# Kernel tuning notes

Measured on AMD Instinct MI355X. Metric: run time of the kernel, lower is better.

The kernel has to match this reference:

```python
import jax, jax.numpy as jnp
import numpy as np

NUM_HEADS = 8
IN_DIM = 384
HEAD_DIM = IN_DIM // NUM_HEADS  # 48


def setup_inputs() -> dict:
    key = jax.random.key(0)
    ks = jax.random.split(key, 6)
    B, N, M, C = 4, 4096, 1024, 384
    q_x = jax.random.normal(ks[0], (B, N, C), dtype=jnp.float32)
    kv_x = jax.random.normal(ks[1], (B, M, C), dtype=jnp.float32)
    s = C ** -0.5  # fan-in style init scale
    Wq = jax.random.normal(ks[2], (C, IN_DIM), dtype=jnp.float32) * s
    Wkv = jax.random.normal(ks[3], (C, 2 * IN_DIM), dtype=jnp.float32) * s
    Wproj = jax.random.normal(ks[4], (IN_DIM, IN_DIM), dtype=jnp.float32) * (IN_DIM ** -0.5)
    bproj = jnp.zeros((IN_DIM,), dtype=jnp.float32)
    return {"q_x": q_x, "kv_x": kv_x, "Wq": Wq, "Wkv": Wkv, "Wproj": Wproj, "bproj": bproj}


def reference(q_x, kv_x, Wq, Wkv, Wproj, bproj):
    B, N, C = q_x.shape
    M = kv_x.shape[1]
    scale = HEAD_DIM ** -0.5
    # q: [B, H, N, hd]
    q = (q_x @ Wq).reshape(B, N, NUM_HEADS, HEAD_DIM).transpose(0, 2, 1, 3)
    # k, v: [B, H, M, hd]
    kv = (kv_x @ Wkv).reshape(B, M, 2, NUM_HEADS, HEAD_DIM).transpose(2, 0, 3, 1, 4)
    k, v = kv[0], kv[1]
    # attention scores [B, H, N, M]
    attn = jax.nn.softmax(jnp.einsum('bhnd,bhmd->bhnm', q, k) * scale, axis=-1)
    x = jnp.einsum('bhnm,bhmd->bhnd', attn, v)  # [B, H, N, hd]
    x = x.transpose(0, 2, 1, 3).reshape(B, N, IN_DIM)
    x = x @ Wproj + bproj
    # sr_ratio == 1 residual: add raw q projection back
    q_res = q.transpose(0, 2, 1, 3).reshape(B, N, IN_DIM)
    return q_res + x
```

## Files before the change

kernel.cpp:

```cpp
#include <hip/hip_runtime.h>
#include <hip/hip_bf16.h>
#include <math.h>

#define B_ 4
#define N_ 4096
#define M_ 1024
#define C_ 384
#define NH_ 8
#define HD_ 48

typedef float f32x4 __attribute__((ext_vector_type(4)));
typedef float f32x16 __attribute__((ext_vector_type(16)));
typedef short bf16x8 __attribute__((ext_vector_type(8)));

typedef __attribute__((address_space(3))) unsigned int lds_uint;
typedef const __attribute__((address_space(1))) unsigned int glob_uint;

__device__ __forceinline__ void gld_lds16(const void* g, void* l) {
    __builtin_amdgcn_global_load_lds((glob_uint*)g, (lds_uint*)l, 16, 0, 0);
}

__device__ __forceinline__ unsigned short f2bf(float x) {
    unsigned int u = __builtin_bit_cast(unsigned int, x);
    return (unsigned short)((u + 0x7FFFu + ((u >> 16) & 1u)) >> 16);
}
__device__ __forceinline__ float bf2f(unsigned short x) {
    return __builtin_bit_cast(float, (unsigned int)x << 16);
}
__device__ __forceinline__ float fast_exp2(float x) {
#if __has_builtin(__builtin_amdgcn_exp2f)
    return __builtin_amdgcn_exp2f(x);
#else
    return exp2f(x);
#endif
}
__device__ __forceinline__ uint2 pack4_rne(float a, float b, float c, float d) {
    uint2 r;
    r.x = (unsigned int)f2bf(a) | ((unsigned int)f2bf(b) << 16);
    r.y = (unsigned int)f2bf(c) | ((unsigned int)f2bf(d) << 16);
    return r;
}

#define QSCALE 0.20823490983597203f
#define INV_QSCALE (1.0f / 0.20823490983597203f)

__global__ __launch_bounds__(256)
void prep(const float* __restrict__ qx_f, unsigned short* __restrict__ qx_bf,
          const float* __restrict__ kvx_f, unsigned short* __restrict__ kvx_bf,
          const float* __restrict__ Wq, const float* __restrict__ Wkv,
          const float* __restrict__ Wproj,
          unsigned short* __restrict__ Wq_t, unsigned short* __restrict__ Wkv_t,
          unsigned short* __restrict__ Wproj_t)
{
    __shared__ unsigned short T[64 * 72];
    const int tid = threadIdx.x;
    int bid = blockIdx.x;

    if (bid < 7680) {
        size_t i4 = (size_t)bid * 256 + tid;
        const float* src; unsigned short* dst;
        if (i4 < 1572864u) { src = qx_f; dst = qx_bf; }
        else { src = kvx_f; dst = kvx_bf; i4 -= 1572864u; }
        float4 v = *(const float4*)&src[i4 * 4];
        *(uint2*)&dst[i4 * 4] = pack4_rne(v.x, v.y, v.z, v.w);
        return;
    }

    bid -= 7680;
    const float* W; unsigned short* Wt; int N, kt, nt;
    if (bid < 36)       { W = Wq;    Wt = Wq_t;    N = 384; kt = bid / 6;  nt = bid - kt * 6; }
    else if (bid < 108) { bid -= 36;  W = Wkv;   Wt = Wkv_t;   N = 768; kt = bid / 12; nt = bid - kt * 12; }
    else                { bid -= 108; W = Wproj; Wt = Wproj_t; N = 384; kt = bid / 6;  nt = bid - kt * 6; }
    const int k0 = kt * 64, n0 = nt * 64;

    #pragma unroll
    for (int it = 0; it < 4; ++it) {
        int k = it * 16 + (tid >> 4);
        int n4 = (tid & 15) * 4;
        float4 v = *(const float4*)&W[(size_t)(k0 + k) * N + n0 + n4];
        T[(n4 + 0) * 72 + k] = f2bf(v.x);
        T[(n4 + 1) * 72 + k] = f2bf(v.y);
        T[(n4 + 2) * 72 + k] = f2bf(v.z);
        T[(n4 + 3) * 72 + k] = f2bf(v.w);
    }
    __syncthreads();
    #pragma unroll
    for (int i = 0; i < 2; ++i) {
        int s = tid + 256 * i;
        int n = s >> 3, part = s & 7;
        *(uint4*)&Wt[(size_t)(n0 + n) * C_ + k0 + part * 8] = *(const uint4*)&T[n * 72 + part * 8];
    }
}

__device__ __forceinline__ void stage128(const unsigned short* src, unsigned short* lds,
                                         int kk, int tid) {
    #pragma unroll
    for (int r = 0; r < 4; ++r) {
        int off = r * 256 + tid;
        int row = off >> 3;
        int c = off & 7;
        int gc = c ^ (row & 7);
        gld_lds16(src + (size_t)row * C_ + kk + gc * 8, lds + (size_t)off * 8);
    }
}
__device__ __forceinline__ bf16x8 frag_ld(const unsigned short* lds, int row, int chunk) {
    return *(const bf16x8*)&lds[row * 64 + ((chunk ^ (row & 7)) << 3)];
}

#define GEMM_CORE(Aptr, Wptr)                                                        \
    f32x4 acc[4][4];                                                                 \
    _Pragma("unroll")                                                                \
    for (int rt = 0; rt < 4; ++rt)                                                   \
        _Pragma("unroll")                                                            \
        for (int ct = 0; ct < 4; ++ct) acc[rt][ct] = (f32x4){0.f, 0.f, 0.f, 0.f};    \
    const int wrow0 = (wave & 1) * 64;                                               \
    const int wcol0 = (wave >> 1) * 64;                                              \
    for (int kk = 0; kk < C_; kk += 64) {                                            \
        __syncthreads();                                                             \
        stage128(Aptr, As, kk, tid);                                                 \
        stage128(Wptr, Ws, kk, tid);                                                 \
        __syncthreads();                                                             \
        _Pragma("unroll")                                                            \
        for (int ks = 0; ks < 2; ++ks) {                                             \
            bf16x8 af[4], wf[4];                                                     \
            _Pragma("unroll")                                                        \
            for (int rt = 0; rt < 4; ++rt)                                           \
                af[rt] = frag_ld(As, wrow0 + rt * 16 + ln, ks * 4 + quad);           \
            _Pragma("unroll")                                                        \
            for (int ct = 0; ct < 4; ++ct)                                           \
                wf[ct] = frag_ld(Ws, wcol0 + ct * 16 + ln, ks * 4 + quad);           \
            _Pragma("unroll")                                                        \
            for (int rt = 0; rt < 4; ++rt)                                           \
                _Pragma("unroll")                                                    \
                for (int ct = 0; ct < 4; ++ct)                                       \
                    acc[rt][ct] = __builtin_amdgcn_mfma_f32_16x16x32_bf16(           \
                        wf[ct], af[rt], acc[rt][ct], 0, 0, 0);                       \
        }                                                                            \
    }

__global__ __launch_bounds__(256)
void gemm_qkv(const unsigned short* __restrict__ qx, const unsigned short* __restrict__ kvx,
              const unsigned short* __restrict__ Wqt, const unsigned short* __restrict__ Wkvt,
              unsigned short* __restrict__ qbf,
              unsigned short* __restrict__ kbf, unsigned short* __restrict__ vbf)
{
    __shared__ unsigned short As[128 * 64];
    __shared__ unsigned short Ws[128 * 64];
    const int tid = threadIdx.x;
    const int wave = tid >> 6;
    const int lane = tid & 63;
    const int ln = lane & 15;
    const int quad = lane >> 4;

    int bid = blockIdx.x;
    int mode, row0, col0;
    const unsigned short *A, *Wt;
    if (bid < 384) { mode = 0; A = qx;  Wt = Wqt;  row0 = (bid / 3) * 128; col0 = (bid % 3) * 128; }
    else { bid -= 384; mode = 1; A = kvx; Wt = Wkvt; row0 = (bid / 6) * 128; col0 = (bid % 6) * 128; }

    GEMM_CORE(A + (size_t)row0 * C_, Wt + (size_t)col0 * C_)

    #pragma unroll
    for (int rt = 0; rt < 4; ++rt) {
        int grow = row0 + wrow0 + rt * 16 + ln;
        #pragma unroll
        for (int ct = 0; ct < 4; ++ct) {
            int col = col0 + wcol0 + ct * 16 + quad * 4;
            f32x4 v = acc[rt][ct];
            if (mode == 0) {
                int b = grow >> 12, n = grow & (N_ - 1);
                int h = col / HD_, d = col - h * HD_;
                *(uint2*)&qbf[(((size_t)(b * NH_ + h) * N_) + n) * HD_ + d] =
                    pack4_rne(v[0] * QSCALE, v[1] * QSCALE, v[2] * QSCALE, v[3] * QSCALE);
            } else {
                int b = grow >> 10, m = grow & (M_ - 1);
                if (col < C_) {
                    int h = col / HD_, d = col - h * HD_;
                    *(uint2*)&kbf[(((size_t)(b * NH_ + h) * M_) + m) * HD_ + d] =
                        pack4_rne(v[0], v[1], v[2], v[3]);
                } else {
                    int c2 = col - C_;
                    int h = c2 / HD_, d = c2 - h * HD_;
                    size_t base = ((size_t)(b * NH_ + h) * HD_ + d) * M_ + m;
                    #pragma unroll
                    for (int r = 0; r < 4; ++r) vbf[base + (size_t)r * M_] = f2bf(v[r]);
                }
            }
        }
    }
}

__global__ __launch_bounds__(256)
void gemm_out(const unsigned short* __restrict__ A, const unsigned short* __restrict__ Wt,
              float* __restrict__ out0,
              const unsigned short* __restrict__ qbf, const float* __restrict__ bias)
{
    __shared__ unsigned short As[128 * 64];
    __shared__ unsigned short Ws[128 * 64];
    const int tid = threadIdx.x;
    const int wave = tid >> 6;
    const int lane = tid & 63;
    const int ln = lane & 15;
    const int quad = lane >> 4;
    const int row0 = (blockIdx.x / 3) * 128;
    const int col0 = (blockIdx.x % 3) * 128;

    GEMM_CORE(A + (size_t)row0 * C_, Wt + (size_t)col0 * C_)

    #pragma unroll
    for (int rt = 0; rt < 4; ++rt) {
        int grow = row0 + wrow0 + rt * 16 + ln;
        #pragma unroll
        for (int ct = 0; ct < 4; ++ct) {
            int col = col0 + wcol0 + ct * 16 + quad * 4;
            f32x4 v = acc[rt][ct];
            size_t idx = (size_t)grow * C_ + col;
            int b = grow >> 12, n = grow & (N_ - 1);
            int h = col / HD_, d = col - h * HD_;
            uint2 ad = *(const uint2*)&qbf[(((size_t)(b * NH_ + h) * N_) + n) * HD_ + d];
            float4 bi = *(const float4*)&bias[col];
            float4 o;
            o.x = v[0] + bf2f((unsigned short)(ad.x & 0xFFFF)) * INV_QSCALE + bi.x;
            o.y = v[1] + bf2f((unsigned short)(ad.x >> 16))    * INV_QSCALE + bi.y;
            o.z = v[2] + bf2f((unsigned short)(ad.y & 0xFFFF)) * INV_QSCALE + bi.z;
            o.w = v[3] + bf2f((unsigned short)(ad.y >> 16))    * INV_QSCALE + bi.w;
            *(float4*)&out0[idx] = o;
        }
    }
}

__global__ __launch_bounds__(256, 2)
void attn_mfma(const unsigned short* __restrict__ qbf,
               const unsigned short* __restrict__ kbf,
               const unsigned short* __restrict__ vbf,
               unsigned short* __restrict__ of)
{
    const int tid = threadIdx.x;
    const int wave = tid >> 6;
    const int lane = tid & 63;
    const int l31 = lane & 31;
    const int hi  = lane >> 5;
    const int bh = blockIdx.x;
    const int n0w = blockIdx.y * 256 + wave * 64;

    const unsigned short* kb = kbf + (size_t)bh * M_ * HD_;
    const unsigned short* vb = vbf + (size_t)bh * HD_ * M_;

    bf16x8 qb[2][3];
    #pragma unroll
    for (int qt = 0; qt < 2; ++qt) {
        const unsigned short* qp = qbf + ((size_t)bh * N_ + n0w + qt * 32 + l31) * HD_;
        #pragma unroll
        for (int s = 0; s < 3; ++s)
            qb[qt][s] = *(const bf16x8*)(qp + s * 16 + hi * 8);
    }

    f32x16 O[2][2];
    #pragma unroll
    for (int qt = 0; qt < 2; ++qt)
        #pragma unroll
        for (int ot2 = 0; ot2 < 2; ++ot2)
            #pragma unroll
            for (int r = 0; r < 16; ++r) O[qt][ot2][r] = 0.f;
    float rs[2] = {0.f, 0.f};

    for (int mtt = 0; mtt < 32; ++mtt) {
        const int m0 = mtt * 32;

        bf16x8 ka[3];
        #pragma unroll
        for (int s = 0; s < 3; ++s)
            ka[s] = *(const bf16x8*)&kb[(size_t)(m0 + l31) * HD_ + s * 16 + hi * 8];

        bf16x8 va[2][2];
        #pragma unroll
        for (int ot2 = 0; ot2 < 2; ++ot2)
            #pragma unroll
            for (int s2 = 0; s2 < 2; ++s2)
                va[ot2][s2] = *(const bf16x8*)&vb[(size_t)(ot2 * 32 + l31) * M_ + m0 + s2 * 16 + hi * 8];

        #pragma unroll
        for (int qt = 0; qt < 2; ++qt) {
            f32x16 S;
            #pragma unroll
            for (int r = 0; r < 16; ++r) S[r] = 0.f;
            #pragma unroll
            for (int s = 0; s < 3; ++s)
                S = __builtin_amdgcn_mfma_f32_32x32x16_bf16(ka[s], qb[qt][s], S, 0, 0, 0);

            float p[16];
            #pragma unroll
            for (int r = 0; r < 16; ++r) p[r] = fast_exp2(S[r]);
            {
                float s0 = (p[0] + p[1]) + (p[2] + p[3]);
                float s1 = (p[4] + p[5]) + (p[6] + p[7]);
                float s2 = (p[8] + p[9]) + (p[10] + p[11]);
                float s3 = (p[12] + p[13]) + (p[14] + p[15]);
                rs[qt] += (s0 + s1) + (s2 + s3);
            }

            unsigned c0[4], c1[4];
            #pragma unroll
            for (int g = 0; g < 4; ++g) {
                c0[g] = (__builtin_bit_cast(unsigned int, p[4 * g + 0]) >> 16) |
                        (__builtin_bit_cast(unsigned int, p[4 * g + 1]) & 0xFFFF0000u);
                c1[g] = (__builtin_bit_cast(unsigned int, p[4 * g + 2]) >> 16) |
                        (__builtin_bit_cast(unsigned int, p[4 * g + 3]) & 0xFFFF0000u);
            }

            #pragma unroll
            for (int s2 = 0; s2 < 2; ++s2) {
                unsigned o00 = c0[2 * s2], o01 = c0[2 * s2 + 1];
                unsigned o10 = c1[2 * s2], o11 = c1[2 * s2 + 1];
                unsigned pr0 = (unsigned)__shfl_xor((int)(hi ? o00 : o01), 32);
                unsigned pr1 = (unsigned)__shfl_xor((int)(hi ? o10 : o11), 32);
                unsigned d0 = hi ? pr0 : o00;
                unsigned d1 = hi ? pr1 : o10;
                unsigned d2 = hi ? o01 : pr0;
                unsigned d3 = hi ? o11 : pr1;
                uint4 u = {d0, d1, d2, d3};
                bf16x8 pf = __builtin_bit_cast(bf16x8, u);
                #pragma unroll
                for (int ot2 = 0; ot2 < 2; ++ot2)
                    O[qt][ot2] = __builtin_amdgcn_mfma_f32_32x32x16_bf16(
                        va[ot2][s2], pf, O[qt][ot2], 0, 0, 0);
            }
        }
    }

    float inv[2];
    #pragma unroll
    for (int qt = 0; qt < 2; ++qt) {
        float x = rs[qt] + __shfl_xor(rs[qt], 32);
        inv[qt] = 1.0f / x;
    }

    const int b = bh >> 3, h = bh & 7;
    #pragma unroll
    for (int qt = 0; qt < 2; ++qt) {
        size_t grow = (size_t)b * N_ + n0w + qt * 32 + l31;
        unsigned short* orow = of + grow * C_ + h * HD_;
        #pragma unroll
        for (int ot2 = 0; ot2 < 2; ++ot2) {
            const int rgmax = (ot2 == 0) ? 4 : 2;
            #pragma unroll
            for (int rg = 0; rg < 4; ++rg) {
                if (rg >= rgmax) continue;
                int d0 = ot2 * 32 + rg * 8 + hi * 4;
                *(uint2*)(orow + d0) = pack4_rne(
                    O[qt][ot2][rg * 4 + 0] * inv[qt], O[qt][ot2][rg * 4 + 1] * inv[qt],
                    O[qt][ot2][rg * 4 + 2] * inv[qt], O[qt][ot2][rg * 4 + 3] * inv[qt]);
            }
        }
    }
}

extern "C" void kernel_launch(void* const* d_in, const int* in_sizes, int n_in,
                              void* d_out, int out_size, void* d_ws, size_t ws_size,
                              hipStream_t stream) {
    const float* q_x   = (const float*)d_in[0];
    const float* kv_x  = (const float*)d_in[1];
    const float* Wq    = (const float*)d_in[2];
    const float* Wkv   = (const float*)d_in[3];
    const float* Wproj = (const float*)d_in[4];
    const float* bproj = (const float*)d_in[5];
    float* out = (float*)d_out;

    unsigned short* qbf     = (unsigned short*)d_ws;
    unsigned short* kbf     = qbf     + 6291456;
    unsigned short* vbf     = kbf     + 1572864;
    unsigned short* of      = vbf     + 1572864;
    unsigned short* qx_bf   = of      + 6291456;
    unsigned short* kvx_bf  = qx_bf   + 6291456;
    unsigned short* Wq_t    = kvx_bf  + 1572864;
    unsigned short* Wkv_t   = Wq_t    + 147456;
    unsigned short* Wproj_t = Wkv_t   + 294912;

    dim3 blk(256);

    prep<<<dim3(7824), blk, 0, stream>>>(q_x, qx_bf, kv_x, kvx_bf,
                                         Wq, Wkv, Wproj, Wq_t, Wkv_t, Wproj_t);

    gemm_qkv<<<dim3(576), blk, 0, stream>>>(
        qx_bf, kvx_bf, Wq_t, Wkv_t, qbf, kbf, vbf);

    attn_mfma<<<dim3(32, 16), blk, 0, stream>>>(qbf, kbf, vbf, of);

    gemm_out<<<dim3(384), blk, 0, stream>>>(of, Wproj_t, out, qbf, bproj);
}
```

Baseline: 168.8 us.

## Double-buffer LDS tiles in projection GEMMs to overlap loads with MFMA

The shared GEMM core used by the QKV and output projections now keeps two LDS buffers for the A and W tiles. The next K-slice is prefetched with global_load_lds while MFMAs run on the current one, and there is one barrier per iteration instead of two. The aim is to hide global-to-LDS latency behind compute. This doubles LDS use per block to 64KB, which may lower occupancy.

```diff
diff --git a/kernel.cpp b/kernel.cpp
--- a/kernel.cpp
+++ b/kernel.cpp
@@ -115,20 +115,25 @@
         for (int ct = 0; ct < 4; ++ct) acc[rt][ct] = (f32x4){0.f, 0.f, 0.f, 0.f};    \
     const int wrow0 = (wave & 1) * 64;                                               \
     const int wcol0 = (wave >> 1) * 64;                                              \
-    for (int kk = 0; kk < C_; kk += 64) {                                            \
-        __syncthreads();                                                             \
-        stage128(Aptr, As, kk, tid);                                                 \
-        stage128(Wptr, Ws, kk, tid);                                                 \
-        __syncthreads();                                                             \
+    stage128(Aptr, &As[0][0], 0, tid);                                               \
+    stage128(Wptr, &Ws[0][0], 0, tid);                                               \
+    asm volatile("s_waitcnt vmcnt(0)" ::: "memory");                                 \
+    __builtin_amdgcn_s_barrier();                                                    \
+    for (int kt = 0; kt < 6; ++kt) {                                                 \
+        const int cur = kt & 1;                                                      \
+        if (kt < 5) {                                                                \
+            stage128(Aptr, &As[cur ^ 1][0], (kt + 1) * 64, tid);                     \
+            stage128(Wptr, &Ws[cur ^ 1][0], (kt + 1) * 64, tid);                     \
+        }                                                                            \
         _Pragma("unroll")                                                            \
         for (int ks = 0; ks < 2; ++ks) {                                             \
             bf16x8 af[4], wf[4];                                                     \
             _Pragma("unroll")                                                        \
             for (int rt = 0; rt < 4; ++rt)                                           \
-                af[rt] = frag_ld(As, wrow0 + rt * 16 + ln, ks * 4 + quad);           \
+                af[rt] = frag_ld(&As[cur][0], wrow0 + rt * 16 + ln, ks * 4 + quad);  \
             _Pragma("unroll")                                                        \
             for (int ct = 0; ct < 4; ++ct)                                           \
-                wf[ct] = frag_ld(Ws, wcol0 + ct * 16 + ln, ks * 4 + quad);           \
+                wf[ct] = frag_ld(&Ws[cur][0], wcol0 + ct * 16 + ln, ks * 4 + quad);  \
             _Pragma("unroll")                                                        \
             for (int rt = 0; rt < 4; ++rt)                                           \
                 _Pragma("unroll")                                                    \
@@ -136,6 +141,10 @@
                     acc[rt][ct] = __builtin_amdgcn_mfma_f32_16x16x32_bf16(           \
                         wf[ct], af[rt], acc[rt][ct], 0, 0, 0);                       \
         }                                                                            \
+        asm volatile("s_waitcnt vmcnt(0)" ::: "memory");                             \
+        __builtin_amdgcn_sched_barrier(0);                                           \
+        __builtin_amdgcn_s_barrier();                                                \
+        __builtin_amdgcn_sched_barrier(0);                                           \
     }
 
 __global__ __launch_bounds__(256)
@@ -144,8 +153,8 @@
               unsigned short* __restrict__ qbf,
               unsigned short* __restrict__ kbf, unsigned short* __restrict__ vbf)
 {
-    __shared__ unsigned short As[128 * 64];
-    __shared__ unsigned short Ws[128 * 64];
+    __shared__ unsigned short As[2][128 * 64];
+    __shared__ unsigned short Ws[2][128 * 64];
     const int tid = threadIdx.x;
     const int wave = tid >> 6;
     const int lane = tid & 63;
@@ -195,8 +204,8 @@
               float* __restrict__ out0,
               const unsigned short* __restrict__ qbf, const float* __restrict__ bias)
 {
-    __shared__ unsigned short As[128 * 64];
-    __shared__ unsigned short Ws[128 * 64];
+    __shared__ unsigned short As[2][128 * 64];
+    __shared__ unsigned short Ws[2][128 * 64];
     const int tid = threadIdx.x;
     const int wave = tid >> 6;
     const int lane = tid & 63;
```

Result: no change. 169.5 us (+0.4%).

## Split attention key range across wave pairs and combine partial outputs in LDS

Applied to the files above, without the earlier changes.

Each attention block now covers 128 queries instead of 256. Two waves share each 64-query tile, and each wave processes half of the 1024 keys. The second wave writes its partial O accumulators and row sums to shared memory, and the first wave adds them in before normalizing. The query range is covered by two back-to-back launches offset by a y0 parameter, and the launch bound is raised to 4 blocks per SM. The aim is to shorten the per-wave serial key loop and raise occupancy, at the cost of an LDS reduction, a block barrier, an extra launch and tighter register limits that could cause spills.

```diff
diff --git a/kernel.cpp b/kernel.cpp
--- a/kernel.cpp
+++ b/kernel.cpp
@@ -229,19 +229,23 @@
     }
 }
 
-__global__ __launch_bounds__(256, 2)
+__global__ __launch_bounds__(256, 4)
 void attn_mfma(const unsigned short* __restrict__ qbf,
                const unsigned short* __restrict__ kbf,
                const unsigned short* __restrict__ vbf,
-               unsigned short* __restrict__ of)
+               unsigned short* __restrict__ of, int y0)
 {
+    __shared__ float comb[2][64][72];
+
     const int tid = threadIdx.x;
     const int wave = tid >> 6;
+    const int qpair = wave >> 1;
+    const int mhalf = wave & 1;
     const int lane = tid & 63;
     const int l31 = lane & 31;
     const int hi  = lane >> 5;
     const int bh = blockIdx.x;
-    const int n0w = blockIdx.y * 256 + wave * 64;
+    const int n0w = (blockIdx.y + y0) * 128 + qpair * 64;
 
     const unsigned short* kb = kbf + (size_t)bh * M_ * HD_;
     const unsigned short* vb = vbf + (size_t)bh * HD_ * M_;
@@ -264,7 +268,8 @@
             for (int r = 0; r < 16; ++r) O[qt][ot2][r] = 0.f;
     float rs[2] = {0.f, 0.f};
 
-    for (int mtt = 0; mtt < 32; ++mtt) {
+    const int mtt0 = mhalf * 16;
+    for (int mtt = mtt0; mtt < mtt0 + 16; ++mtt) {
         const int m0 = mtt * 32;
 
         bf16x8 ka[3];
@@ -328,6 +333,29 @@
         }
     }
 
+    if (mhalf) {
+        float* ex = &comb[qpair][lane][0];
+        *(f32x16*)&ex[0]  = O[0][0];
+        *(f32x16*)&ex[16] = O[0][1];
+        *(f32x16*)&ex[32] = O[1][0];
+        *(f32x16*)&ex[48] = O[1][1];
+        ex[64] = rs[0];
+        ex[65] = rs[1];
+    }
+    __syncthreads();
+    if (mhalf) return;
+
+    {
+        const float* ex = &comb[qpair][lane][0];
+        f32x16 u00 = *(const f32x16*)&ex[0];
+        f32x16 u01 = *(const f32x16*)&ex[16];
+        f32x16 u10 = *(const f32x16*)&ex[32];
+        f32x16 u11 = *(const f32x16*)&ex[48];
+        O[0][0] += u00; O[0][1] += u01; O[1][0] += u10; O[1][1] += u11;
+        rs[0] += ex[64];
+        rs[1] += ex[65];
+    }
+
     float inv[2];
     #pragma unroll
     for (int qt = 0; qt < 2; ++qt) {
@@ -384,7 +412,8 @@
     gemm_qkv<<<dim3(576), blk, 0, stream>>>(
         qx_bf, kvx_bf, Wq_t, Wkv_t, qbf, kbf, vbf);
 
-    attn_mfma<<<dim3(32, 16), blk, 0, stream>>>(qbf, kbf, vbf, of);
+    attn_mfma<<<dim3(32, 16), blk, 0, stream>>>(qbf, kbf, vbf, of, 0);
+    attn_mfma<<<dim3(32, 16), blk, 0, stream>>>(qbf, kbf, vbf, of, 16);
 
     gemm_out<<<dim3(384), blk, 0, stream>>>(of, Wproj_t, out, qbf, bproj);
 }
```

After: 353.1 us. 2.09x slower.

## Double-buffer K/V loads in attention and halve output GEMM column tile

Applied to the files above, without the earlier changes.

The attention loop now prefetches the next 32-key K/V fragment set into registers while computing the current one, ping-ponging between two register buffers, and wraps the MFMA groups in s_setprio to favour matrix issue. The output projection GEMM switches from 128x128 to 128x64 tiles, doubling the grid to 768 blocks for better CU occupancy. The costs are extra register pressure in attention, which may hurt occupancy at the 2-block launch bound, and more redundant A-tile loads in the output GEMM.

```diff
diff --git a/kernel.cpp b/kernel.cpp
--- a/kernel.cpp
+++ b/kernel.cpp
@@ -96,6 +96,17 @@
                                          int kk, int tid) {
     #pragma unroll
     for (int r = 0; r < 4; ++r) {
+        int off = r * 256 + tid;
+        int row = off >> 3;
+        int c = off & 7;
+        int gc = c ^ (row & 7);
+        gld_lds16(src + (size_t)row * C_ + kk + gc * 8, lds + (size_t)off * 8);
+    }
+}
+__device__ __forceinline__ void stage64(const unsigned short* src, unsigned short* lds,
+                                        int kk, int tid) {
+    #pragma unroll
+    for (int r = 0; r < 2; ++r) {
         int off = r * 256 + tid;
         int row = off >> 3;
         int c = off & 7;
@@ -196,22 +207,53 @@
               const unsigned short* __restrict__ qbf, const float* __restrict__ bias)
 {
     __shared__ unsigned short As[128 * 64];
-    __shared__ unsigned short Ws[128 * 64];
+    __shared__ unsigned short Ws[64 * 64];
     const int tid = threadIdx.x;
     const int wave = tid >> 6;
     const int lane = tid & 63;
     const int ln = lane & 15;
     const int quad = lane >> 4;
-    const int row0 = (blockIdx.x / 3) * 128;
-    const int col0 = (blockIdx.x % 3) * 128;
-
-    GEMM_CORE(A + (size_t)row0 * C_, Wt + (size_t)col0 * C_)
+    const int row0 = (blockIdx.x / 6) * 128;
+    const int col0 = (blockIdx.x % 6) * 64;
+    const int wrow0 = (wave & 1) * 64;
+    const int wcol0 = (wave >> 1) * 32;
+
+    f32x4 acc[4][2];
+    #pragma unroll
+    for (int rt = 0; rt < 4; ++rt)
+        #pragma unroll
+        for (int ct = 0; ct < 2; ++ct) acc[rt][ct] = (f32x4){0.f, 0.f, 0.f, 0.f};
+
+    const unsigned short* Ap = A + (size_t)row0 * C_;
+    const unsigned short* Wp = Wt + (size_t)col0 * C_;
+    for (int kk = 0; kk < C_; kk += 64) {
+        __syncthreads();
+        stage128(Ap, As, kk, tid);
+        stage64(Wp, Ws, kk, tid);
+        __syncthreads();
+        #pragma unroll
+        for (int ks = 0; ks < 2; ++ks) {
+            bf16x8 af[4], wf[2];
+            #pragma unroll
+            for (int rt = 0; rt < 4; ++rt)
+                af[rt] = frag_ld(As, wrow0 + rt * 16 + ln, ks * 4 + quad);
+            #pragma unroll
+            for (int ct = 0; ct < 2; ++ct)
+                wf[ct] = frag_ld(Ws, wcol0 + ct * 16 + ln, ks * 4 + quad);
+            #pragma unroll
+            for (int rt = 0; rt < 4; ++rt)
+                #pragma unroll
+                for (int ct = 0; ct < 2; ++ct)
+                    acc[rt][ct] = __builtin_amdgcn_mfma_f32_16x16x32_bf16(
+                        wf[ct], af[rt], acc[rt][ct], 0, 0, 0);
+        }
+    }
 
     #pragma unroll
     for (int rt = 0; rt < 4; ++rt) {
         int grow = row0 + wrow0 + rt * 16 + ln;
         #pragma unroll
-        for (int ct = 0; ct < 4; ++ct) {
+        for (int ct = 0; ct < 2; ++ct) {
             int col = col0 + wcol0 + ct * 16 + quad * 4;
             f32x4 v = acc[rt][ct];
             size_t idx = (size_t)grow * C_ + col;
@@ -229,6 +271,78 @@
     }
 }
 
+__device__ __forceinline__ void attn_load(bf16x8 (&ka)[3], bf16x8 (&va)[2][2],
+                                          const unsigned short* kb,
+                                          const unsigned short* vb,
+                                          int m0, int l31, int hi)
+{
+    #pragma unroll
+    for (int s = 0; s < 3; ++s)
+        ka[s] = *(const bf16x8*)&kb[(size_t)(m0 + l31) * HD_ + s * 16 + hi * 8];
+    #pragma unroll
+    for (int ot2 = 0; ot2 < 2; ++ot2)
+        #pragma unroll
+        for (int s2 = 0; s2 < 2; ++s2)
+            va[ot2][s2] = *(const bf16x8*)&vb[(size_t)(ot2 * 32 + l31) * M_ + m0 + s2 * 16 + hi * 8];
+}
+
+__device__ __forceinline__ void attn_compute(const bf16x8 (&ka)[3], const bf16x8 (&va)[2][2],
+                                             const bf16x8 (&qb)[2][3],
+                                             f32x16 (&O)[2][2], float (&rs)[2], int hi)
+{
+    #pragma unroll
+    for (int qt = 0; qt < 2; ++qt) {
+        f32x16 S;
+        #pragma unroll
+        for (int r = 0; r < 16; ++r) S[r] = 0.f;
+        __builtin_amdgcn_s_setprio(1);
+        #pragma unroll
+        for (int s = 0; s < 3; ++s)
+            S = __builtin_amdgcn_mfma_f32_32x32x16_bf16(ka[s], qb[qt][s], S, 0, 0, 0);
+        __builtin_amdgcn_s_setprio(0);
+
+        float p[16];
+        #pragma unroll
+        for (int r = 0; r < 16; ++r) p[r] = fast_exp2(S[r]);
+        {
+            float s0 = (p[0] + p[1]) + (p[2] + p[3]);
+            float s1 = (p[4] + p[5]) + (p[6] + p[7]);
+            float s2 = (p[8] + p[9]) + (p[10] + p[11]);
+            float s3 = (p[12] + p[13]) + (p[14] + p[15]);
+            rs[qt] += (s0 + s1) + (s2 + s3);
+        }
+
+        unsigned c0[4], c1[4];
+        #pragma unroll
+        for (int g = 0; g < 4; ++g) {
+            c0[g] = (__builtin_bit_cast(unsigned int, p[4 * g + 0]) >> 16) |
+                    (__builtin_bit_cast(unsigned int, p[4 * g + 1]) & 0xFFFF0000u);
+            c1[g] = (__builtin_bit_cast(unsigned int, p[4 * g + 2]) >> 16) |
+                    (__builtin_bit_cast(unsigned int, p[4 * g + 3]) & 0xFFFF0000u);
+        }
+
+        #pragma unroll
+        for (int s2 = 0; s2 < 2; ++s2) {
+            unsigned o00 = c0[2 * s2], o01 = c0[2 * s2 + 1];
+            unsigned o10 = c1[2 * s2], o11 = c1[2 * s2 + 1];
+            unsigned pr0 = (unsigned)__shfl_xor((int)(hi ? o00 : o01), 32);
+            unsigned pr1 = (unsigned)__shfl_xor((int)(hi ? o10 : o11), 32);
+            unsigned d0 = hi ? pr0 : o00;
+            unsigned d1 = hi ? pr1 : o10;
+            unsigned d2 = hi ? o01 : pr0;
+            unsigned d3 = hi ? o11 : pr1;
+            uint4 u = {d0, d1, d2, d3};
+            bf16x8 pf = __builtin_bit_cast(bf16x8, u);
+            __builtin_amdgcn_s_setprio(1);
+            #pragma unroll
+            for (int ot2 = 0; ot2 < 2; ++ot2)
+                O[qt][ot2] = __builtin_amdgcn_mfma_f32_32x32x16_bf16(
+                    va[ot2][s2], pf, O[qt][ot2], 0, 0, 0);
+            __builtin_amdgcn_s_setprio(0);
+        }
+    }
+}
+
 __global__ __launch_bounds__(256, 2)
 void attn_mfma(const unsigned short* __restrict__ qbf,
                const unsigned short* __restrict__ kbf,
@@ -264,68 +378,15 @@
             for (int r = 0; r < 16; ++r) O[qt][ot2][r] = 0.f;
     float rs[2] = {0.f, 0.f};
 
-    for (int mtt = 0; mtt < 32; ++mtt) {
-        const int m0 = mtt * 32;
-
-        bf16x8 ka[3];
-        #pragma unroll
-        for (int s = 0; s < 3; ++s)
-            ka[s] = *(const bf16x8*)&kb[(size_t)(m0 + l31) * HD_ + s * 16 + hi * 8];
-
-        bf16x8 va[2][2];
-        #pragma unroll
-        for (int ot2 = 0; ot2 < 2; ++ot2)
-            #pragma unroll
-            for (int s2 = 0; s2 < 2; ++s2)
-                va[ot2][s2] = *(const bf16x8*)&vb[(size_t)(ot2 * 32 + l31) * M_ + m0 + s2 * 16 + hi * 8];
-
-        #pragma unroll
-        for (int qt = 0; qt < 2; ++qt) {
-            f32x16 S;
-            #pragma unroll
-            for (int r = 0; r < 16; ++r) S[r] = 0.f;
-            #pragma unroll
-            for (int s = 0; s < 3; ++s)
-                S = __builtin_amdgcn_mfma_f32_32x32x16_bf16(ka[s], qb[qt][s], S, 0, 0, 0);
-
-            float p[16];
-            #pragma unroll
-            for (int r = 0; r < 16; ++r) p[r] = fast_exp2(S[r]);
-            {
-                float s0 = (p[0] + p[1]) + (p[2] + p[3]);
-                float s1 = (p[4] + p[5]) + (p[6] + p[7]);
-                float s2 = (p[8] + p[9]) + (p[10] + p[11]);
-                float s3 = (p[12] + p[13]) + (p[14] + p[15]);
-                rs[qt] += (s0 + s1) + (s2 + s3);
-            }
-
-            unsigned c0[4], c1[4];
-            #pragma unroll
-            for (int g = 0; g < 4; ++g) {
-                c0[g] = (__builtin_bit_cast(unsigned int, p[4 * g + 0]) >> 16) |
-                        (__builtin_bit_cast(unsigned int, p[4 * g + 1]) & 0xFFFF0000u);
-                c1[g] = (__builtin_bit_cast(unsigned int, p[4 * g + 2]) >> 16) |
-                        (__builtin_bit_cast(unsigned int, p[4 * g + 3]) & 0xFFFF0000u);
-            }
-
-            #pragma unroll
-            for (int s2 = 0; s2 < 2; ++s2) {
-                unsigned o00 = c0[2 * s2], o01 = c0[2 * s2 + 1];
-                unsigned o10 = c1[2 * s2], o11 = c1[2 * s2 + 1];
-                unsigned pr0 = (unsigned)__shfl_xor((int)(hi ? o00 : o01), 32);
-                unsigned pr1 = (unsigned)__shfl_xor((int)(hi ? o10 : o11), 32);
-                unsigned d0 = hi ? pr0 : o00;
-                unsigned d1 = hi ? pr1 : o10;
-                unsigned d2 = hi ? o01 : pr0;
-                unsigned d3 = hi ? o11 : pr1;
-                uint4 u = {d0, d1, d2, d3};
-                bf16x8 pf = __builtin_bit_cast(bf16x8, u);
-                #pragma unroll
-                for (int ot2 = 0; ot2 < 2; ++ot2)
-                    O[qt][ot2] = __builtin_amdgcn_mfma_f32_32x32x16_bf16(
-                        va[ot2][s2], pf, O[qt][ot2], 0, 0, 0);
-            }
-        }
+    bf16x8 kaA[3], vaA[2][2], kaB[3], vaB[2][2];
+    attn_load(kaA, vaA, kb, vb, 0, l31, hi);
+
+    for (int mtt = 0; mtt < 32; mtt += 2) {
+        attn_load(kaB, vaB, kb, vb, (mtt + 1) * 32, l31, hi);
+        attn_compute(kaA, vaA, qb, O, rs, hi);
+        if (mtt + 2 < 32)
+            attn_load(kaA, vaA, kb, vb, (mtt + 2) * 32, l31, hi);
+        attn_compute(kaB, vaB, qb, O, rs, hi);
     }
 
     float inv[2];
@@ -386,5 +447,5 @@
 
     attn_mfma<<<dim3(32, 16), blk, 0, stream>>>(qbf, kbf, vbf, of);
 
-    gemm_out<<<dim3(384), blk, 0, stream>>>(of, Wproj_t, out, qbf, bproj);
-}
+    gemm_out<<<dim3(768), blk, 0, stream>>>(of, Wproj_t, out, qbf, bproj);
+}
```

After: 168.6 us. No clear change (-0.1%).
